# Optimization experiments

Hardware: AMD Instinct MI355X
Metric: run time of the kernel (lower is better)

The kernel has to match this reference:

```python
import jax, jax.numpy as jnp
import numpy as np

LN_EPS = 1e-7

def gelu(x):
    # BERT erf-based gelu
    return 0.5 * x * (1.0 + jax.lax.erf(x / jnp.sqrt(2.0).astype(x.dtype)))

def setup_inputs() -> dict:
    key = jax.random.key(0)
    k1, k2 = jax.random.split(key)
    B, S, H, I = 4, 4096, 1024, 4096
    hidden_states = jax.random.normal(k1, (B, S, H), dtype=jnp.float32)
    W = jax.random.normal(k2, (H, I), dtype=jnp.float32) * (1.0 / np.sqrt(H))
    b = jnp.zeros((I,), dtype=jnp.float32)
    ln_gamma = jnp.ones((H,), dtype=jnp.float32)
    ln_beta = jnp.zeros((H,), dtype=jnp.float32)
    return {"hidden_states": hidden_states, "ln_gamma": ln_gamma, "ln_beta": ln_beta, "W": W, "b": b}

def reference(hidden_states, ln_gamma, ln_beta, W, b):
    # LayerNorm over last dim
    mu = jnp.mean(hidden_states, axis=-1, keepdims=True)
    xc = hidden_states - mu
    var = jnp.mean(xc * xc, axis=-1, keepdims=True)
    x_norm = xc * jax.lax.rsqrt(var + LN_EPS) * ln_gamma + ln_beta
    # Linear projection [B,S,H] @ [H,I] + b, then gelu
    y = jnp.einsum('bsh,hi->bsi', x_norm, W) + b
    return gelu(y)
```

## Files before the change

kernel.cpp:

```cpp
#include <hip/hip_runtime.h>
#include <hip/hip_bf16.h>

typedef __attribute__((ext_vector_type(8))) short bf16x8;
typedef __attribute__((ext_vector_type(4))) float f32x4;

static __device__ __forceinline__ unsigned short f2bf(float f) {
    unsigned u = __builtin_bit_cast(unsigned, f);
    unsigned rounding = 0x7fffu + ((u >> 16) & 1u);
    u += rounding;
    return (unsigned short)(u >> 16);
}

static __device__ __forceinline__ void async_copy16(const void* g, void* l) {
    __builtin_amdgcn_global_load_lds(
        (const __attribute__((address_space(1))) unsigned int*)g,
        (__attribute__((address_space(3))) unsigned int*)l,
        16, 0, 0);
}

#define BARRIER() __builtin_amdgcn_s_barrier()
#define VM0()    do { asm volatile("s_waitcnt vmcnt(0)" ::: "memory"); \
                      __builtin_amdgcn_sched_barrier(0); } while (0)

static __device__ __forceinline__ float fast_gelu(float y) {
    float u = 0.7978845608028654f * y * (1.0f + 0.044715f * y * y);
    float au = fminf(fabsf(u), 9.0f);
    float e = __expf(-2.0f * au);
    float th = (1.0f - e) * __builtin_amdgcn_rcpf(1.0f + e);
    th = (u < 0.0f) ? -th : th;
    return 0.5f * y * (1.0f + th);
}

__global__ __launch_bounds__(256) void ln_cast_kernel(
    const float* __restrict__ x, const float* __restrict__ gamma,
    const float* __restrict__ beta, unsigned short* __restrict__ out) {
    const int row = blockIdx.x;
    const int t = threadIdx.x;
    const float4 v = ((const float4*)(x + (size_t)row * 1024))[t];

    float s  = v.x + v.y + v.z + v.w;
    float ss = v.x * v.x + v.y * v.y + v.z * v.z + v.w * v.w;
    #pragma unroll
    for (int off = 32; off; off >>= 1) {
        s  += __shfl_down(s, off);
        ss += __shfl_down(ss, off);
    }
    __shared__ float red[8];
    const int wid = t >> 6, lane = t & 63;
    if (lane == 0) { red[wid] = s; red[wid + 4] = ss; }
    __syncthreads();
    if (t == 0) {
        float S  = red[0] + red[1] + red[2] + red[3];
        float SS = red[4] + red[5] + red[6] + red[7];
        float mu = S * (1.0f / 1024.0f);
        float var = SS * (1.0f / 1024.0f) - mu * mu;
        red[0] = mu;
        red[1] = rsqrtf(var + 1e-7f);
    }
    __syncthreads();
    const float mu = red[0], rs = red[1];
    const float4 g = ((const float4*)gamma)[t];
    const float4 b = ((const float4*)beta)[t];

    ushort4 pk;
    pk.x = f2bf((v.x - mu) * rs * g.x + b.x);
    pk.y = f2bf((v.y - mu) * rs * g.y + b.y);
    pk.z = f2bf((v.z - mu) * rs * g.z + b.z);
    pk.w = f2bf((v.w - mu) * rs * g.w + b.w);
    ((ushort4*)(out + (size_t)row * 1024))[t] = pk;
}

__global__ __launch_bounds__(256) void wt_cast_kernel(
    const float* __restrict__ W, unsigned short* __restrict__ Wt) {
    __shared__ float tile[32][33];
    const int bx = blockIdx.x;
    const int by = blockIdx.y;
    const int tx = threadIdx.x & 31;
    const int ty = threadIdx.x >> 5;
    #pragma unroll
    for (int i = 0; i < 4; ++i) {
        int k = by * 32 + ty + i * 8;
        tile[ty + i * 8][tx] = W[(size_t)k * 4096 + bx * 32 + tx];
    }
    __syncthreads();
    #pragma unroll
    for (int i = 0; i < 4; ++i) {
        int n = bx * 32 + ty + i * 8;
        Wt[(size_t)n * 1024 + by * 32 + tx] = f2bf(tile[tx][ty + i * 8]);
    }
}

__global__ __launch_bounds__(256, 2) void gemm_kernel(
    const unsigned short* __restrict__ A, const unsigned short* __restrict__ Wt,
    const float* __restrict__ bias, float* __restrict__ out) {
    __shared__ char lds_mem[65536];

    const int bid = blockIdx.x;
    const int swz = (bid & 7) * 512 + (bid >> 3);
    const int bm = swz >> 5;
    const int bn = swz & 31;

    const int t = threadIdx.x;
    const int lane = t & 63;
    const int wid = t >> 6;
    const int wm = wid >> 1, wn = wid & 1;
    const int lrow = lane & 15;
    const int lk = lane >> 4;

    const int srr = t >> 3;
    const int sch = t & 7;
    const int sgc = sch ^ (srr & 7);
    const unsigned short* gA = A  + (size_t)(bm * 128 + srr) * 1024 + sgc * 8;
    const unsigned short* gB = Wt + (size_t)(bn * 128 + srr) * 1024 + sgc * 8;
    const int lst = srr * 128 + sch * 16;

    auto stage = [&](int kt, char* buf) {
        #pragma unroll
        for (int i = 0; i < 4; ++i) {
            async_copy16(gA + (size_t)(i * 32) * 1024 + kt * 64, buf + i * 32 * 128 + lst);
            async_copy16(gB + (size_t)(i * 32) * 1024 + kt * 64, buf + 16384 + i * 32 * 128 + lst);
        }
    };

    const int ck0 = ((lk) ^ (lrow & 7)) * 16;
    const int ck1 = ((4 + lk) ^ (lrow & 7)) * 16;
    const int aBase = (wm * 64 + lrow) * 128;
    const int bBase = 16384 + (wn * 64 + lrow) * 128;

    f32x4 acc[4][4];
    #pragma unroll
    for (int i = 0; i < 4; ++i)
        #pragma unroll
        for (int j = 0; j < 4; ++j) acc[i][j] = (f32x4)0.0f;

    float bv[4];
    #pragma unroll
    for (int ni = 0; ni < 4; ++ni) bv[ni] = bias[bn * 128 + wn * 64 + ni * 16 + lrow];

    stage(0, lds_mem);
    VM0();
    BARRIER();

    const int NKT = 16;
    for (int kt = 0; kt < NKT; ++kt) {
        char* cbuf = lds_mem + ((kt & 1) << 15);
        char* nbuf = lds_mem + (((kt + 1) & 1) << 15);

        bf16x8 af[4][2], bf[4][2];
        #pragma unroll
        for (int mi = 0; mi < 4; ++mi) {
            const char* p = cbuf + aBase + mi * 16 * 128;
            af[mi][0] = *(const bf16x8*)(p + ck0);
            af[mi][1] = *(const bf16x8*)(p + ck1);
        }
        #pragma unroll
        for (int ni = 0; ni < 4; ++ni) {
            const char* p = cbuf + bBase + ni * 16 * 128;
            bf[ni][0] = *(const bf16x8*)(p + ck0);
            bf[ni][1] = *(const bf16x8*)(p + ck1);
        }

        if (kt + 1 < NKT) stage(kt + 1, nbuf);

        __builtin_amdgcn_s_setprio(1);
        #pragma unroll
        for (int mi = 0; mi < 4; ++mi)
            #pragma unroll
            for (int ni = 0; ni < 4; ++ni) {
                acc[mi][ni] = __builtin_amdgcn_mfma_f32_16x16x32_bf16(af[mi][0], bf[ni][0], acc[mi][ni], 0, 0, 0);
                acc[mi][ni] = __builtin_amdgcn_mfma_f32_16x16x32_bf16(af[mi][1], bf[ni][1], acc[mi][ni], 0, 0, 0);
            }
        __builtin_amdgcn_s_setprio(0);

        if (kt + 1 < NKT) {
            VM0();
            BARRIER();
        }
    }

    #pragma unroll
    for (int mi = 0; mi < 4; ++mi) {
        const int row0 = bm * 128 + wm * 64 + mi * 16 + lk * 4;
        #pragma unroll
        for (int ni = 0; ni < 4; ++ni) {
            const int col = bn * 128 + wn * 64 + ni * 16 + lrow;
            #pragma unroll
            for (int r = 0; r < 4; ++r) {
                float y = acc[mi][ni][r] + bv[ni];
                out[(size_t)(row0 + r) * 4096 + col] = fast_gelu(y);
            }
        }
    }
}

extern "C" void kernel_launch(void* const* d_in, const int* in_sizes, int n_in,
                              void* d_out, int out_size, void* d_ws, size_t ws_size,
                              hipStream_t stream) {
    const float* hidden = (const float*)d_in[0];
    const float* gamma  = (const float*)d_in[1];
    const float* beta   = (const float*)d_in[2];
    const float* W      = (const float*)d_in[3];
    const float* bias   = (const float*)d_in[4];
    float* out = (float*)d_out;

    unsigned short* Abf = (unsigned short*)d_ws;
    unsigned short* Wt  = (unsigned short*)((char*)d_ws + (size_t)16384 * 1024 * 2);

    ln_cast_kernel<<<16384, 256, 0, stream>>>(hidden, gamma, beta, Abf);
    wt_cast_kernel<<<dim3(128, 32), 256, 0, stream>>>(W, Wt);
    gemm_kernel<<<4096, 256, 0, stream>>>(Abf, Wt, bias, out);
}
```

Before: 214.7 us.

## Load B operand directly from global into registers, halve LDS for occupancy

The weight tile is no longer staged through LDS. Each wave loads its B fragments straight from global memory into double-buffered registers one k-step ahead, while A stays in LDS. This halves LDS use to 32KB, and launch bounds are raised to 3 blocks per CU to gain occupancy. The trade-off is that the two waves sharing a B tile fetch it redundantly from global/L2, and the extra register buffers may push up register pressure under the tighter launch bound.

```diff
diff --git a/kernel.cpp b/kernel.cpp
--- a/kernel.cpp
+++ b/kernel.cpp
@@ -90,10 +90,10 @@
     }
 }
 
-__global__ __launch_bounds__(256, 2) void gemm_kernel(
+__global__ __launch_bounds__(256, 3) void gemm_kernel(
     const unsigned short* __restrict__ A, const unsigned short* __restrict__ Wt,
     const float* __restrict__ bias, float* __restrict__ out) {
-    __shared__ char lds_mem[65536];
+    __shared__ char lds_mem[32768];
 
     const int bid = blockIdx.x;
     const int swz = (bid & 7) * 512 + (bid >> 3);
@@ -110,22 +110,28 @@
     const int srr = t >> 3;
     const int sch = t & 7;
     const int sgc = sch ^ (srr & 7);
-    const unsigned short* gA = A  + (size_t)(bm * 128 + srr) * 1024 + sgc * 8;
-    const unsigned short* gB = Wt + (size_t)(bn * 128 + srr) * 1024 + sgc * 8;
+    const unsigned short* gA = A + (size_t)(bm * 128 + srr) * 1024 + sgc * 8;
     const int lst = srr * 128 + sch * 16;
 
     auto stage = [&](int kt, char* buf) {
         #pragma unroll
-        for (int i = 0; i < 4; ++i) {
+        for (int i = 0; i < 4; ++i)
             async_copy16(gA + (size_t)(i * 32) * 1024 + kt * 64, buf + i * 32 * 128 + lst);
-            async_copy16(gB + (size_t)(i * 32) * 1024 + kt * 64, buf + 16384 + i * 32 * 128 + lst);
+    };
+
+    const unsigned short* gBw = Wt + (size_t)(bn * 128 + wn * 64 + lrow) * 1024 + lk * 8;
+    auto loadB = [&](int kt, bf16x8 (*b)[2]) {
+        #pragma unroll
+        for (int ni = 0; ni < 4; ++ni) {
+            const unsigned short* p = gBw + (size_t)(ni * 16) * 1024 + kt * 64;
+            b[ni][0] = *(const bf16x8*)(p);
+            b[ni][1] = *(const bf16x8*)(p + 32);
         }
     };
 
     const int ck0 = ((lk) ^ (lrow & 7)) * 16;
     const int ck1 = ((4 + lk) ^ (lrow & 7)) * 16;
     const int aBase = (wm * 64 + lrow) * 128;
-    const int bBase = 16384 + (wn * 64 + lrow) * 128;
 
     f32x4 acc[4][4];
     #pragma unroll
@@ -137,46 +143,49 @@
     #pragma unroll
     for (int ni = 0; ni < 4; ++ni) bv[ni] = bias[bn * 128 + wn * 64 + ni * 16 + lrow];
 
+    bf16x8 bf0[4][2], bf1[4][2];
+
+    loadB(0, bf0);
     stage(0, lds_mem);
     VM0();
     BARRIER();
 
-    const int NKT = 16;
-    for (int kt = 0; kt < NKT; ++kt) {
-        char* cbuf = lds_mem + ((kt & 1) << 15);
-        char* nbuf = lds_mem + (((kt + 1) & 1) << 15);
-
-        bf16x8 af[4][2], bf[4][2];
+    auto body = [&](int kt, char* cbuf, char* nbuf, bf16x8 (*bcur)[2],
+                    bf16x8 (*bnext)[2], bool notLast) {
+        bf16x8 af[4][2];
         #pragma unroll
         for (int mi = 0; mi < 4; ++mi) {
             const char* p = cbuf + aBase + mi * 16 * 128;
             af[mi][0] = *(const bf16x8*)(p + ck0);
             af[mi][1] = *(const bf16x8*)(p + ck1);
         }
-        #pragma unroll
-        for (int ni = 0; ni < 4; ++ni) {
-            const char* p = cbuf + bBase + ni * 16 * 128;
-            bf[ni][0] = *(const bf16x8*)(p + ck0);
-            bf[ni][1] = *(const bf16x8*)(p + ck1);
-        }
-
-        if (kt + 1 < NKT) stage(kt + 1, nbuf);
-
+        if (notLast) {
+            loadB(kt + 1, bnext);
+            stage(kt + 1, nbuf);
+        }
         __builtin_amdgcn_s_setprio(1);
         #pragma unroll
         for (int mi = 0; mi < 4; ++mi)
             #pragma unroll
             for (int ni = 0; ni < 4; ++ni) {
-                acc[mi][ni] = __builtin_amdgcn_mfma_f32_16x16x32_bf16(af[mi][0], bf[ni][0], acc[mi][ni], 0, 0, 0);
-                acc[mi][ni] = __builtin_amdgcn_mfma_f32_16x16x32_bf16(af[mi][1], bf[ni][1], acc[mi][ni], 0, 0, 0);
+                acc[mi][ni] = __builtin_amdgcn_mfma_f32_16x16x32_bf16(af[mi][0], bcur[ni][0], acc[mi][ni], 0, 0, 0);
+                acc[mi][ni] = __builtin_amdgcn_mfma_f32_16x16x32_bf16(af[mi][1], bcur[ni][1], acc[mi][ni], 0, 0, 0);
             }
         __builtin_amdgcn_s_setprio(0);
-
-        if (kt + 1 < NKT) {
+        if (notLast) {
             VM0();
             BARRIER();
         }
-    }
+    };
+
+    char* lds0 = lds_mem;
+    char* lds1 = lds_mem + 16384;
+    for (int kt2 = 0; kt2 < 7; ++kt2) {
+        body(2 * kt2,     lds0, lds1, bf0, bf1, true);
+        body(2 * kt2 + 1, lds1, lds0, bf1, bf0, true);
+    }
+    body(14, lds0, lds1, bf0, bf1, true);
+    body(15, lds1, lds0, bf1, bf0, false);
 
     #pragma unroll
     for (int mi = 0; mi < 4; ++mi) {
```

Measured after the change: 458.6 us. +113.6%, slower.
